# Optimization experiments

Hardware: AMD Instinct MI355X
Metric: run time of the kernel (lower is better)

The kernel has to match this reference:

```python
import jax, jax.numpy as jnp
import numpy as np

N_ENT = 100000
N_REL = 237
IN_DIM = 128
OUT_DIM = 128
E = 400000


def setup_inputs() -> dict:
    key = jax.random.key(0)
    k1, k2, k3, k4, k5, k6, k7, k8 = jax.random.split(key, 8)
    src = jax.random.randint(k1, (E,), 0, N_ENT)
    dst = jax.random.randint(k2, (E,), 0, N_ENT)
    rel = jax.random.randint(k3, (E,), 0, N_REL)
    triplets = jnp.stack([src, dst, rel], axis=1)  # [E, 3]
    ent_embed = jax.random.normal(k4, (N_ENT, IN_DIM), dtype=jnp.float32)
    rel_embed = jax.random.normal(k5, (N_REL, IN_DIM), dtype=jnp.float32)
    # xavier_normal with gain=1.414 for weights; torch Linear bias ~ U(-1/sqrt(fan_in), 1/sqrt(fan_in))
    g = 1.414
    Wa = jax.random.normal(k6, (OUT_DIM, 3 * IN_DIM), dtype=jnp.float32) * (g * np.sqrt(2.0 / (3 * IN_DIM + OUT_DIM)))
    ba = jnp.zeros((OUT_DIM,), dtype=jnp.float32)
    Wa2 = jax.random.normal(k7, (1, OUT_DIM), dtype=jnp.float32) * (g * np.sqrt(2.0 / (OUT_DIM + 1)))
    ba2 = jnp.zeros((1,), dtype=jnp.float32)
    return {"triplets": triplets, "ent_embed": ent_embed, "rel_embed": rel_embed,
            "Wa": Wa, "ba": ba, "Wa2": Wa2, "ba2": ba2}


def reference(triplets, ent_embed, rel_embed, Wa, ba, Wa2, ba2):
    src, dst, rel = triplets[:, 0], triplets[:, 1], triplets[:, 2]
    # per-edge feature: [E, 3*in_dim]
    h = jnp.concatenate([ent_embed[src], rel_embed[rel], ent_embed[dst]], axis=1)
    c = h @ Wa.T + ba                                  # [E, out_dim]
    b = jax.nn.leaky_relu(c @ Wa2.T + ba2)             # [E, 1], slope 0.01
    e_b = jnp.exp(b)                                   # [E, 1]
    # segment-sum over source nodes (torch.sparse.sum over dim=1 of [N,N,F])
    e_b_sum = jax.ops.segment_sum(e_b, src, num_segments=N_ENT)       # [N, 1]
    temp1 = e_b * c                                    # [E, out_dim]
    h_sum = jax.ops.segment_sum(temp1, src, num_segments=N_ENT)       # [N, out_dim]
    ebs = jnp.where(e_b_sum == 0, 1e-12, e_b_sum)
    h_ent = h_sum / ebs                                # [N, out_dim]
    # scatter-mean of temp1 by relation id
    rel_sum = jax.ops.segment_sum(temp1, rel, num_segments=N_REL)     # [R, out_dim]
    rel_cnt = jax.ops.segment_sum(jnp.ones((temp1.shape[0], 1), temp1.dtype), rel, num_segments=N_REL)
    h_rel = rel_sum / jnp.maximum(rel_cnt, 1.0)        # [R, out_dim]
    return jax.nn.elu(h_ent), jax.nn.elu(h_rel)
```

## Files before the change

### kernel.cpp

```cpp
#include <hip/hip_runtime.h>
#include <math.h>

#define N_ENT 100000
#define N_REL 237
#define DIM   128
#define NE    400000
#define SEGB  ((N_ENT + 15) / 16)

typedef short bf16x8 __attribute__((ext_vector_type(8)));
typedef float f32x4  __attribute__((ext_vector_type(4)));


__device__ __forceinline__ unsigned short f2bf(float f) {
    unsigned int u = __float_as_uint(f);
    u += 0x7FFF + ((u >> 16) & 1);
    return (unsigned short)(u >> 16);
}

__global__ void k_wah(const float* __restrict__ Wa, unsigned short* __restrict__ Wah) {
    int i = blockIdx.x * 256 + threadIdx.x;
    if (i < 128 * 384) Wah[i] = f2bf(Wa[i]);
}

__global__ void k_vsd(const float* __restrict__ Wa, const float* __restrict__ Wa2,
                      float* __restrict__ vs, float* __restrict__ vd) {
    int t = threadIdx.x;
    if (t < 128) {
        float a = 0.f;
        for (int j = 0; j < 128; ++j) a += Wa[j * 384 + t] * Wa2[j];
        vs[t] = a;
    } else if (t < 256) {
        int k = t - 128;
        float a = 0.f;
        for (int j = 0; j < 128; ++j) a += Wa[j * 384 + 256 + k] * Wa2[j];
        vd[k] = a;
    }
}

__global__ void k_proj_rel(const float* __restrict__ rel_e, const float* __restrict__ Wa,
                           const float* __restrict__ ba, float* __restrict__ Pr) {
    int i = blockIdx.x * 256 + threadIdx.x;
    if (i >= N_REL * DIM) return;
    int r = i >> 7, j = i & 127;
    float acc = ba[j];
    const float* wrow = Wa + j * 384 + 128;
    const float* erow = rel_e + r * DIM;
    #pragma unroll 8
    for (int k = 0; k < DIM; ++k) acc += erow[k] * wrow[k];
    Pr[i] = acc;
}

__global__ void k_qr(const float* __restrict__ Pr, const float* __restrict__ Wa2,
                     const float* __restrict__ ba2, float* __restrict__ qr) {
    const int lane = threadIdx.x & 63;
    const int r = (blockIdx.x * 256 + threadIdx.x) >> 6;
    if (r >= N_REL) return;
    float p = Pr[r * DIM + lane] * Wa2[lane] + Pr[r * DIM + 64 + lane] * Wa2[64 + lane];
    #pragma unroll
    for (int off = 32; off > 0; off >>= 1) p += __shfl_xor(p, off, 64);
    if (lane == 0) qr[r] = p + ba2[0];
}

__global__ __launch_bounds__(256) void k_proj_mfma(const float* __restrict__ ent,
        const unsigned short* __restrict__ Wah,
        const float* __restrict__ vs, const float* __restrict__ vd,
        float* __restrict__ Ps, float* __restrict__ Pd,
        float* __restrict__ qs, float* __restrict__ qd) {
    const int wave = threadIdx.x >> 6, lane = threadIdx.x & 63;
    const int row0 = blockIdx.x * 64 + wave * 16;
    const int lr = lane & 15;
    const int lg = lane >> 4;
    const int arow = (row0 + lr < N_ENT) ? row0 + lr : (N_ENT - 1);

    f32x4 accS[8], accD[8];
    #pragma unroll
    for (int t = 0; t < 8; ++t) {
        accS[t] = (f32x4){0.f, 0.f, 0.f, 0.f};
        accD[t] = (f32x4){0.f, 0.f, 0.f, 0.f};
    }
    float qsp = 0.f, qdp = 0.f;

    #pragma unroll
    for (int kk = 0; kk < 4; ++kk) {
        const int k0 = kk * 32 + lg * 8;
        const float* ep = ent + (size_t)arow * DIM + k0;
        float4 e0 = *(const float4*)ep;
        float4 e1 = *(const float4*)(ep + 4);
        float4 v0 = *(const float4*)(vs + k0);
        float4 v1 = *(const float4*)(vs + k0 + 4);
        qsp += e0.x*v0.x + e0.y*v0.y + e0.z*v0.z + e0.w*v0.w
             + e1.x*v1.x + e1.y*v1.y + e1.z*v1.z + e1.w*v1.w;
        float4 u0 = *(const float4*)(vd + k0);
        float4 u1 = *(const float4*)(vd + k0 + 4);
        qdp += e0.x*u0.x + e0.y*u0.y + e0.z*u0.z + e0.w*u0.w
             + e1.x*u1.x + e1.y*u1.y + e1.z*u1.z + e1.w*u1.w;
        bf16x8 a;
        a[0] = (short)f2bf(e0.x); a[1] = (short)f2bf(e0.y);
        a[2] = (short)f2bf(e0.z); a[3] = (short)f2bf(e0.w);
        a[4] = (short)f2bf(e1.x); a[5] = (short)f2bf(e1.y);
        a[6] = (short)f2bf(e1.z); a[7] = (short)f2bf(e1.w);
        #pragma unroll
        for (int t = 0; t < 8; ++t) {
            const size_t wb = (size_t)(t * 16 + lr) * 384 + k0;
            bf16x8 bs = *(const bf16x8*)(Wah + wb);
            bf16x8 bd = *(const bf16x8*)(Wah + wb + 256);
            accS[t] = __builtin_amdgcn_mfma_f32_16x16x32_bf16(a, bs, accS[t], 0, 0, 0);
            accD[t] = __builtin_amdgcn_mfma_f32_16x16x32_bf16(a, bd, accD[t], 0, 0, 0);
        }
    }

    #pragma unroll
    for (int q = 0; q < 4; ++q) {
        const int row = row0 + lg * 4 + q;
        if (row < N_ENT) {
            #pragma unroll
            for (int t = 0; t < 8; ++t) {
                Ps[(size_t)row * DIM + t * 16 + lr] = accS[t][q];
                Pd[(size_t)row * DIM + t * 16 + lr] = accD[t][q];
            }
        }
    }

    qsp += __shfl_xor(qsp, 16, 64); qsp += __shfl_xor(qsp, 32, 64);
    qdp += __shfl_xor(qdp, 16, 64); qdp += __shfl_xor(qdp, 32, 64);
    if (lane < 16 && row0 + lane < N_ENT) {
        qs[row0 + lane] = qsp;
        qd[row0 + lane] = qdp;
    }
}

__global__ void k_hist2(const int* __restrict__ trip, int* __restrict__ scnt,
                        int* __restrict__ rcnt) {
    __shared__ int lh[N_REL];
    for (int i = threadIdx.x; i < N_REL; i += 256) lh[i] = 0;
    __syncthreads();
    int e0 = blockIdx.x * 1024 + threadIdx.x * 4;
    #pragma unroll
    for (int k = 0; k < 4; ++k) {
        int e = e0 + k;
        if (e < NE) {
            atomicAdd(scnt + trip[3 * e], 1);
            atomicAdd(&lh[trip[3 * e + 2]], 1);
        }
    }
    __syncthreads();
    for (int i = threadIdx.x; i < N_REL; i += 256)
        if (lh[i]) atomicAdd(rcnt + i, lh[i]);
}

__global__ void k_scan1(const int* __restrict__ cnt, int* __restrict__ escan,
                        int* __restrict__ bsum) {
    __shared__ int sh[256];
    const int t = threadIdx.x;
    int base = blockIdx.x * 1024 + t * 4;
    int v[4]; int s = 0;
    #pragma unroll
    for (int k = 0; k < 4; ++k) { int idx = base + k; v[k] = (idx < N_ENT) ? cnt[idx] : 0; s += v[k]; }
    sh[t] = s; __syncthreads();
    for (int off = 1; off < 256; off <<= 1) {
        int u = (t >= off) ? sh[t - off] : 0;
        __syncthreads();
        sh[t] += u;
        __syncthreads();
    }
    int run = sh[t] - s;
    #pragma unroll
    for (int k = 0; k < 4; ++k) { int idx = base + k; if (idx < N_ENT) escan[idx] = run; run += v[k]; }
    if (t == 255) bsum[blockIdx.x] = sh[255];
}

__global__ void k_scan2(int* __restrict__ bsum) {
    __shared__ int sh[128];
    const int t = threadIdx.x;
    int v = (t < 98) ? bsum[t] : 0;
    sh[t] = v; __syncthreads();
    for (int off = 1; off < 128; off <<= 1) {
        int u = (t >= off) ? sh[t - off] : 0;
        __syncthreads();
        sh[t] += u;
        __syncthreads();
    }
    if (t < 98) bsum[t] = sh[t] - v;
}

__global__ void k_scan3(int* __restrict__ row_start, const int* __restrict__ bsum,
                        int* __restrict__ cursor) {
    int i = blockIdx.x * 256 + threadIdx.x;
    if (i < N_ENT) {
        int v = row_start[i] + bsum[i >> 10];
        row_start[i] = v;
        cursor[i] = v;
    } else if (i == N_ENT) {
        row_start[N_ENT] = NE;
    }
}

__global__ void k_relscan(const int* __restrict__ rcnt, int* __restrict__ rrow,
                          int* __restrict__ rcursor) {
    __shared__ int sh[256];
    const int t = threadIdx.x;
    int v = (t < N_REL) ? rcnt[t] : 0;
    sh[t] = v; __syncthreads();
    for (int off = 1; off < 256; off <<= 1) {
        int u = (t >= off) ? sh[t - off] : 0;
        __syncthreads();
        sh[t] += u;
        __syncthreads();
    }
    int excl = sh[t] - v;
    if (t <= N_REL) rrow[t] = excl;
    if (t < N_REL) rcursor[t] = excl;
}

__global__ __launch_bounds__(256) void k_scatter3(const int* __restrict__ trip,
        int* __restrict__ scursor, int* __restrict__ rcursor,
        int2* __restrict__ sdr, int2* __restrict__ rsd) {
    __shared__ int lh[N_REL];
    __shared__ int lbase[N_REL];
    const int t = threadIdx.x;
    for (int i = t; i < N_REL; i += 256) lh[i] = 0;
    __syncthreads();

    const int e0 = blockIdx.x * 1024 + t * 4;
    int sv[4], dv[4], rv[4];
    #pragma unroll
    for (int k = 0; k < 4; ++k) {
        int e = e0 + k;
        if (e < NE) {
            sv[k] = trip[3 * e]; dv[k] = trip[3 * e + 1]; rv[k] = trip[3 * e + 2];
            atomicAdd(&lh[rv[k]], 1);
        } else { sv[k] = -1; }
    }
    __syncthreads();
    for (int i = t; i < N_REL; i += 256) {
        int c = lh[i];
        lbase[i] = c ? atomicAdd(rcursor + i, c) : 0;
        lh[i] = 0;
    }
    __syncthreads();
    #pragma unroll
    for (int k = 0; k < 4; ++k) {
        if (sv[k] >= 0) {
            int p1 = atomicAdd(scursor + sv[k], 1);
            sdr[p1] = make_int2(dv[k], rv[k]);
            int intra = atomicAdd(&lh[rv[k]], 1);
            rsd[lbase[rv[k]] + intra] = make_int2(sv[k], dv[k]);
        }
    }
}

__global__ __launch_bounds__(1024) void k_edges(const int* __restrict__ rrow,
        const int2* __restrict__ rsd,
        const int* __restrict__ row_start, const int2* __restrict__ sdr,
        const float* __restrict__ Ps, const float* __restrict__ Pd, const float* __restrict__ Pr,
        const float* __restrict__ qs, const float* __restrict__ qd, const float* __restrict__ qr,
        float* __restrict__ out) {
    __shared__ float red[16 * 128];
    __shared__ float reb[16];
    const int t = threadIdx.x;
    const int lane = t & 63;

    if (blockIdx.x < N_REL) {
        const int r = blockIdx.x;
        const int w = t >> 6;
        const float myqr = qr[r];
        const int beg = rrow[r], end = rrow[r + 1];
        float a0 = 0.f, a1 = 0.f, ebs = 0.f;
        for (int j = beg + w; j < end; j += 16) {
            int2 sd = rsd[j];
            float b = myqr + qs[sd.x] + qd[sd.y];
            b = (b > 0.f) ? b : 0.01f * b;
            float eb = expf(b);
            a0 += eb * (Ps[(size_t)sd.x * DIM + lane]      + Pd[(size_t)sd.y * DIM + lane]);
            a1 += eb * (Ps[(size_t)sd.x * DIM + 64 + lane] + Pd[(size_t)sd.y * DIM + 64 + lane]);
            ebs += eb;
        }
        red[w * 128 + lane]      = a0;
        red[w * 128 + 64 + lane] = a1;
        if (lane == 0) reb[w] = ebs;
        __syncthreads();
        if (t < 128) {
            float ssum = 0.f, et = 0.f;
            #pragma unroll
            for (int ww = 0; ww < 16; ++ww) { ssum += red[ww * 128 + t]; et += reb[ww]; }
            float h = (ssum + et * Pr[r * DIM + t]) / fmaxf((float)(end - beg), 1.0f);
            out[(size_t)N_ENT * DIM + r * DIM + t] = (h > 0.f) ? h : expm1f(h);
        }
    } else {
        const int s = (blockIdx.x - N_REL) * 16 + (t >> 6);
        if (s >= N_ENT) return;
        const int beg = row_start[s], end = row_start[s + 1];
        if (beg == end) {
            out[(size_t)s * DIM + lane] = 0.f;
            out[(size_t)s * DIM + 64 + lane] = 0.f;
            return;
        }
        const float myqs = qs[s];
        float acc0 = 0.f, acc1 = 0.f, ebs = 0.f;
        for (int j = beg; j < end; ++j) {
            int2 dr = sdr[j];
            float b = myqs + qr[dr.y] + qd[dr.x];
            b = (b > 0.f) ? b : 0.01f * b;
            float eb = expf(b);
            acc0 += eb * (Pr[dr.y * DIM + lane]      + Pd[(size_t)dr.x * DIM + lane]);
            acc1 += eb * (Pr[dr.y * DIM + 64 + lane] + Pd[(size_t)dr.x * DIM + 64 + lane]);
            ebs += eb;
        }
        float h0 = Ps[(size_t)s * DIM + lane]      + acc0 / ebs;
        float h1 = Ps[(size_t)s * DIM + 64 + lane] + acc1 / ebs;
        out[(size_t)s * DIM + lane]      = (h0 > 0.f) ? h0 : expm1f(h0);
        out[(size_t)s * DIM + 64 + lane] = (h1 > 0.f) ? h1 : expm1f(h1);
    }
}

extern "C" void kernel_launch(void* const* d_in, const int* in_sizes, int n_in,
                              void* d_out, int out_size, void* d_ws, size_t ws_size,
                              hipStream_t stream) {
    const int*   trip = (const int*)d_in[0];
    const float* ent  = (const float*)d_in[1];
    const float* rele = (const float*)d_in[2];
    const float* Wa   = (const float*)d_in[3];
    const float* ba   = (const float*)d_in[4];
    const float* Wa2  = (const float*)d_in[5];
    const float* ba2  = (const float*)d_in[6];
    float* out = (float*)d_out;

    float* ws  = (float*)d_ws;
    float* Ps  = ws;
    float* Pd  = Ps + (size_t)N_ENT * DIM;
    float* Pr  = Pd + (size_t)N_ENT * DIM;
    float* qs  = Pr + N_REL * DIM;
    float* qd  = qs + N_ENT;
    float* qr  = qd + N_ENT;
    float* vs  = qr + 240;
    float* vd  = vs + 128;
    unsigned short* Wah = (unsigned short*)(vd + 128);
    int* row_start = (int*)(vd + 128 + 24576);
    int* cursor    = row_start + N_ENT + 1;
    int* rcnt      = cursor + N_ENT;
    int* rrow      = rcnt + 240;
    int* rcursor   = rrow + 240;
    int* bsum      = rcursor + 240;
    int2* sdr      = (int2*)(bsum + 128);
    int2* rsd      = sdr + NE;

    hipMemsetAsync(cursor, 0, (N_ENT + 240) * sizeof(int), stream);

    k_wah<<<192, 256, 0, stream>>>(Wa, Wah);
    k_vsd<<<1, 256, 0, stream>>>(Wa, Wa2, vs, vd);
    k_proj_rel<<<(N_REL * DIM + 255) / 256, 256, 0, stream>>>(rele, Wa, ba, Pr);
    k_qr<<<(N_REL * 64 + 255) / 256, 256, 0, stream>>>(Pr, Wa2, ba2, qr);
    k_proj_mfma<<<(N_ENT + 63) / 64, 256, 0, stream>>>(ent, Wah, vs, vd, Ps, Pd, qs, qd);

    k_hist2<<<(NE + 1023) / 1024, 256, 0, stream>>>(trip, cursor, rcnt);
    k_scan1<<<98, 256, 0, stream>>>(cursor, row_start, bsum);
    k_scan2<<<1, 128, 0, stream>>>(bsum);
    k_scan3<<<(N_ENT + 256) / 256, 256, 0, stream>>>(row_start, bsum, cursor);
    k_relscan<<<1, 256, 0, stream>>>(rcnt, rrow, rcursor);
    k_scatter3<<<(NE + 1023) / 1024, 256, 0, stream>>>(trip, cursor, rcursor, sdr, rsd);

    k_edges<<<N_REL + SEGB, 1024, 0, stream>>>(rrow, rsd, row_start, sdr,
                                               Ps, Pd, Pr, qs, qd, qr, out);
}
```

Measured before the change: 389.6 us.

## Store projected embeddings in bf16 and merge small prep kernels

The per-entity projections Ps/Pd and the relation projection are now written as bf16, so the edge-gather kernel reads half as many bytes per edge. The feature layout per lane changes to adjacent pairs, loaded as one 32-bit word and unpacked into two floats. The four small setup kernels are also folded into two launches. This adds rounding error to the aggregated features and may risk tolerance, in exchange for less gather bandwidth and fewer launches.

```diff
diff --git a/kernel.cpp b/kernel.cpp
--- a/kernel.cpp
+++ b/kernel.cpp
@@ -16,55 +16,56 @@
     u += 0x7FFF + ((u >> 16) & 1);
     return (unsigned short)(u >> 16);
 }
-
-__global__ void k_wah(const float* __restrict__ Wa, unsigned short* __restrict__ Wah) {
-    int i = blockIdx.x * 256 + threadIdx.x;
-    if (i < 128 * 384) Wah[i] = f2bf(Wa[i]);
-}
-
-__global__ void k_vsd(const float* __restrict__ Wa, const float* __restrict__ Wa2,
-                      float* __restrict__ vs, float* __restrict__ vd) {
-    int t = threadIdx.x;
-    if (t < 128) {
-        float a = 0.f;
-        for (int j = 0; j < 128; ++j) a += Wa[j * 384 + t] * Wa2[j];
-        vs[t] = a;
-    } else if (t < 256) {
-        int k = t - 128;
-        float a = 0.f;
-        for (int j = 0; j < 128; ++j) a += Wa[j * 384 + 256 + k] * Wa2[j];
-        vd[k] = a;
-    }
-}
-
-__global__ void k_proj_rel(const float* __restrict__ rel_e, const float* __restrict__ Wa,
-                           const float* __restrict__ ba, float* __restrict__ Pr) {
-    int i = blockIdx.x * 256 + threadIdx.x;
-    if (i >= N_REL * DIM) return;
-    int r = i >> 7, j = i & 127;
+__device__ __forceinline__ float bflo(unsigned int v) { return __uint_as_float(v << 16); }
+__device__ __forceinline__ float bfhi(unsigned int v) { return __uint_as_float(v & 0xffff0000u); }
+
+__global__ void k_prep0(const float* __restrict__ Wa, unsigned short* __restrict__ Wah,
+                        const float* __restrict__ Wa2, float* __restrict__ vs,
+                        float* __restrict__ vd) {
+    if (blockIdx.x < 192) {
+        int i = blockIdx.x * 256 + threadIdx.x;
+        if (i < 128 * 384) Wah[i] = f2bf(Wa[i]);
+    } else {
+        int t = threadIdx.x;
+        if (t < 128) {
+            float a = 0.f;
+            for (int j = 0; j < 128; ++j) a += Wa[j * 384 + t] * Wa2[j];
+            vs[t] = a;
+        } else {
+            int k = t - 128;
+            float a = 0.f;
+            for (int j = 0; j < 128; ++j) a += Wa[j * 384 + 256 + k] * Wa2[j];
+            vd[k] = a;
+        }
+    }
+}
+
+__global__ void k_prep_rel(const float* __restrict__ rel_e, const float* __restrict__ Wa,
+                           const float* __restrict__ ba, const float* __restrict__ Wa2,
+                           const float* __restrict__ ba2, float* __restrict__ Pr,
+                           unsigned short* __restrict__ Prh, float* __restrict__ qr) {
+    __shared__ float sred[128];
+    const int r = blockIdx.x, j = threadIdx.x;
     float acc = ba[j];
     const float* wrow = Wa + j * 384 + 128;
     const float* erow = rel_e + r * DIM;
     #pragma unroll 8
     for (int k = 0; k < DIM; ++k) acc += erow[k] * wrow[k];
-    Pr[i] = acc;
-}
-
-__global__ void k_qr(const float* __restrict__ Pr, const float* __restrict__ Wa2,
-                     const float* __restrict__ ba2, float* __restrict__ qr) {
-    const int lane = threadIdx.x & 63;
-    const int r = (blockIdx.x * 256 + threadIdx.x) >> 6;
-    if (r >= N_REL) return;
-    float p = Pr[r * DIM + lane] * Wa2[lane] + Pr[r * DIM + 64 + lane] * Wa2[64 + lane];
-    #pragma unroll
-    for (int off = 32; off > 0; off >>= 1) p += __shfl_xor(p, off, 64);
-    if (lane == 0) qr[r] = p + ba2[0];
+    Pr[r * DIM + j]  = acc;
+    Prh[r * DIM + j] = f2bf(acc);
+    sred[j] = acc * Wa2[j];
+    __syncthreads();
+    for (int off = 64; off > 0; off >>= 1) {
+        if (j < off) sred[j] += sred[j + off];
+        __syncthreads();
+    }
+    if (j == 0) qr[r] = sred[0] + ba2[0];
 }
 
 __global__ __launch_bounds__(256) void k_proj_mfma(const float* __restrict__ ent,
         const unsigned short* __restrict__ Wah,
         const float* __restrict__ vs, const float* __restrict__ vd,
-        float* __restrict__ Ps, float* __restrict__ Pd,
+        unsigned short* __restrict__ Psh, unsigned short* __restrict__ Pdh,
         float* __restrict__ qs, float* __restrict__ qd) {
     const int wave = threadIdx.x >> 6, lane = threadIdx.x & 63;
     const int row0 = blockIdx.x * 64 + wave * 16;
@@ -115,8 +116,8 @@
         if (row < N_ENT) {
             #pragma unroll
             for (int t = 0; t < 8; ++t) {
-                Ps[(size_t)row * DIM + t * 16 + lr] = accS[t][q];
-                Pd[(size_t)row * DIM + t * 16 + lr] = accD[t][q];
+                Psh[(size_t)row * DIM + t * 16 + lr] = f2bf(accS[t][q]);
+                Pdh[(size_t)row * DIM + t * 16 + lr] = f2bf(accD[t][q]);
             }
         }
     }
@@ -252,13 +253,15 @@
 __global__ __launch_bounds__(1024) void k_edges(const int* __restrict__ rrow,
         const int2* __restrict__ rsd,
         const int* __restrict__ row_start, const int2* __restrict__ sdr,
-        const float* __restrict__ Ps, const float* __restrict__ Pd, const float* __restrict__ Pr,
+        const unsigned short* __restrict__ Psh, const unsigned short* __restrict__ Pdh,
+        const unsigned short* __restrict__ Prh, const float* __restrict__ Pr,
         const float* __restrict__ qs, const float* __restrict__ qd, const float* __restrict__ qr,
         float* __restrict__ out) {
     __shared__ float red[16 * 128];
     __shared__ float reb[16];
     const int t = threadIdx.x;
     const int lane = t & 63;
+    const int dl = 2 * lane;
 
     if (blockIdx.x < N_REL) {
         const int r = blockIdx.x;
@@ -271,12 +274,13 @@
             float b = myqr + qs[sd.x] + qd[sd.y];
             b = (b > 0.f) ? b : 0.01f * b;
             float eb = expf(b);
-            a0 += eb * (Ps[(size_t)sd.x * DIM + lane]      + Pd[(size_t)sd.y * DIM + lane]);
-            a1 += eb * (Ps[(size_t)sd.x * DIM + 64 + lane] + Pd[(size_t)sd.y * DIM + 64 + lane]);
+            unsigned int ps = *(const unsigned int*)(Psh + (size_t)sd.x * DIM + dl);
+            unsigned int pd = *(const unsigned int*)(Pdh + (size_t)sd.y * DIM + dl);
+            a0 += eb * (bflo(ps) + bflo(pd));
+            a1 += eb * (bfhi(ps) + bfhi(pd));
             ebs += eb;
         }
-        red[w * 128 + lane]      = a0;
-        red[w * 128 + 64 + lane] = a1;
+        *(float2*)(red + w * 128 + dl) = make_float2(a0, a1);
         if (lane == 0) reb[w] = ebs;
         __syncthreads();
         if (t < 128) {
@@ -291,8 +295,7 @@
         if (s >= N_ENT) return;
         const int beg = row_start[s], end = row_start[s + 1];
         if (beg == end) {
-            out[(size_t)s * DIM + lane] = 0.f;
-            out[(size_t)s * DIM + 64 + lane] = 0.f;
+            *(float2*)(out + (size_t)s * DIM + dl) = make_float2(0.f, 0.f);
             return;
         }
         const float myqs = qs[s];
@@ -302,14 +305,18 @@
             float b = myqs + qr[dr.y] + qd[dr.x];
             b = (b > 0.f) ? b : 0.01f * b;
             float eb = expf(b);
-            acc0 += eb * (Pr[dr.y * DIM + lane]      + Pd[(size_t)dr.x * DIM + lane]);
-            acc1 += eb * (Pr[dr.y * DIM + 64 + lane] + Pd[(size_t)dr.x * DIM + 64 + lane]);
+            unsigned int pr = *(const unsigned int*)(Prh + (size_t)dr.y * DIM + dl);
+            unsigned int pd = *(const unsigned int*)(Pdh + (size_t)dr.x * DIM + dl);
+            acc0 += eb * (bflo(pr) + bflo(pd));
+            acc1 += eb * (bfhi(pr) + bfhi(pd));
             ebs += eb;
         }
-        float h0 = Ps[(size_t)s * DIM + lane]      + acc0 / ebs;
-        float h1 = Ps[(size_t)s * DIM + 64 + lane] + acc1 / ebs;
-        out[(size_t)s * DIM + lane]      = (h0 > 0.f) ? h0 : expm1f(h0);
-        out[(size_t)s * DIM + 64 + lane] = (h1 > 0.f) ? h1 : expm1f(h1);
+        unsigned int ps = *(const unsigned int*)(Psh + (size_t)s * DIM + dl);
+        float h0 = bflo(ps) + acc0 / ebs;
+        float h1 = bfhi(ps) + acc1 / ebs;
+        h0 = (h0 > 0.f) ? h0 : expm1f(h0);
+        h1 = (h1 > 0.f) ? h1 : expm1f(h1);
+        *(float2*)(out + (size_t)s * DIM + dl) = make_float2(h0, h1);
     }
 }
 
@@ -326,16 +333,17 @@
     float* out = (float*)d_out;
 
     float* ws  = (float*)d_ws;
-    float* Ps  = ws;
-    float* Pd  = Ps + (size_t)N_ENT * DIM;
-    float* Pr  = Pd + (size_t)N_ENT * DIM;
+    float* Pr  = ws;
     float* qs  = Pr + N_REL * DIM;
     float* qd  = qs + N_ENT;
     float* qr  = qd + N_ENT;
     float* vs  = qr + 240;
     float* vd  = vs + 128;
-    unsigned short* Wah = (unsigned short*)(vd + 128);
-    int* row_start = (int*)(vd + 128 + 24576);
+    unsigned short* Psh = (unsigned short*)(vd + 128);
+    unsigned short* Pdh = Psh + (size_t)N_ENT * DIM;
+    unsigned short* Prh = Pdh + (size_t)N_ENT * DIM;
+    unsigned short* Wah = Prh + N_REL * DIM;
+    int* row_start = (int*)(Wah + 128 * 384);
     int* cursor    = row_start + N_ENT + 1;
     int* rcnt      = cursor + N_ENT;
     int* rrow      = rcnt + 240;
@@ -346,11 +354,10 @@
 
     hipMemsetAsync(cursor, 0, (N_ENT + 240) * sizeof(int), stream);
 
-    k_wah<<<192, 256, 0, stream>>>(Wa, Wah);
-    k_vsd<<<1, 256, 0, stream>>>(Wa, Wa2, vs, vd);
-    k_proj_rel<<<(N_REL * DIM + 255) / 256, 256, 0, stream>>>(rele, Wa, ba, Pr);
-    k_qr<<<(N_REL * 64 + 255) / 256, 256, 0, stream>>>(Pr, Wa2, ba2, qr);
-    k_proj_mfma<<<(N_ENT + 63) / 64, 256, 0, stream>>>(ent, Wah, vs, vd, Ps, Pd, qs, qd);
+    k_prep0<<<193, 256, 0, stream>>>(Wa, Wah, Wa2, vs, vd);
+    k_prep_rel<<<N_REL, 128, 0, stream>>>(rele, Wa, ba, Wa2, ba2, Pr, Prh, qr);
+    k_proj_mfma<<<(N_ENT + 63) / 64, 256, 0, stream>>>(ent, Wah, vs, vd,
+                                                       Psh, Pdh, qs, qd);
 
     k_hist2<<<(NE + 1023) / 1024, 256, 0, stream>>>(trip, cursor, rcnt);
     k_scan1<<<98, 256, 0, stream>>>(cursor, row_start, bsum);
@@ -360,5 +367,5 @@
     k_scatter3<<<(NE + 1023) / 1024, 256, 0, stream>>>(trip, cursor, rcursor, sdr, rsd);
 
     k_edges<<<N_REL + SEGB, 1024, 0, stream>>>(rrow, rsd, row_start, sdr,
-                                               Ps, Pd, Pr, qs, qd, qr, out);
-}
+                                               Psh, Pdh, Prh, Pr, qs, qd, qr, out);
+}
```

Result: faster. 375.7 us (-3.6%).
